# Kernel tuning notes

Measured on AMD Instinct MI355X. Metric: run time of the kernel, lower is better.

Reference implementation:

```python
import jax, jax.numpy as jnp
import numpy as np

B, C, K, N = 16, 512, 64, 8192
STAGE_NUM = 3


def setup_inputs() -> dict:
    key = jax.random.key(0)
    k0, k1, k2, k3 = jax.random.split(key, 4)
    x = jax.random.normal(k0, (B, C, N), jnp.float32)
    # conv1: Conv1d(c, c, 1) with bias; weight init N(0, sqrt(2/c))
    w1 = jax.random.normal(k1, (C, C), jnp.float32) * np.float32(np.sqrt(2.0 / C))
    b1 = jnp.zeros((C,), jnp.float32)
    # conv2: Conv1d(c, c, 1, bias=False) + BatchNorm1d(c) (gamma=1, beta=0)
    w2 = jax.random.normal(k2, (C, C), jnp.float32) * np.float32(np.sqrt(2.0 / C))
    gamma = jnp.ones((C,), jnp.float32)
    beta = jnp.zeros((C,), jnp.float32)
    # mu buffer: (1, c, k), N(0, sqrt(2/k)); is_normalized=False so no l2norm
    mu0 = jax.random.normal(k3, (1, C, K), jnp.float32) * np.float32(np.sqrt(2.0 / K))
    return {"x": x, "w1": w1, "b1": b1, "mu0": mu0, "w2": w2, "gamma": gamma, "beta": beta}


def reference(x, w1, b1, mu0, w2, gamma, beta):
    idn = x                                             # B,C,N
    # conv1 (1x1 conv == per-point matmul)
    x1 = jnp.einsum('oc,bcn->bon', w1, x) + b1[None, :, None]
    # EM iterations run under torch.no_grad() -> stop_gradient
    xs = jax.lax.stop_gradient(x1)
    mu = jnp.broadcast_to(mu0, (x.shape[0], C, K))      # B,C,K (buffer, no grad)
    z = None
    for _ in range(STAGE_NUM):
        z = jax.nn.softmax(jnp.einsum('bcn,bck->bnk', xs, mu), axis=2)  # E-step
        z_ = z / (1e-6 + z.sum(axis=1, keepdims=True))                  # normalize over N
        mu = jnp.einsum('bcn,bnk->bck', xs, z_)                         # M-step
        # is_normalized=False -> _l2norm is identity
    # reconstruction: mu @ z^T, relu
    x2 = jax.nn.relu(jnp.einsum('bck,bnk->bcn', mu, z))
    # conv2 (1x1, no bias) + BatchNorm1d (training-mode batch stats, eps=1e-5)
    x3 = jnp.einsum('oc,bcn->bon', w2, x2)
    mean = x3.mean(axis=(0, 2), keepdims=True)
    var = x3.var(axis=(0, 2), keepdims=True)
    y = gamma[None, :, None] * (x3 - mean) * jax.lax.rsqrt(var + 1e-5) + beta[None, :, None]
    out = y + idn
    return (out, mu)
```

## Files before the change

kernel.cpp:

```cpp
#include <hip/hip_runtime.h>
#include <math.h>

constexpr int B_ = 16, C_ = 512, K_ = 64, N_ = 8192;
constexpr int BHALF = 8;
constexpr int BGRP = 8;
constexpr int MCHUNK = 512;

typedef __bf16 bf16;
typedef __bf16 bf16x4 __attribute__((ext_vector_type(4)));
typedef __bf16 bf16x8 __attribute__((ext_vector_type(8)));
typedef float f32x4 __attribute__((ext_vector_type(4)));

#define GLDS16(gp, lp)                                              \
  __builtin_amdgcn_global_load_lds(                                 \
      (const __attribute__((address_space(1))) unsigned int*)(gp),  \
      (__attribute__((address_space(3))) unsigned int*)(lp), 16, 0, 0)

__device__ __forceinline__ bf16 lo_part(float v, bf16 h) {
  return (bf16)(v - (float)h);
}

__global__ __launch_bounds__(256) void transpose_split_x(
    const float* __restrict__ X, bf16* __restrict__ XTH, bf16* __restrict__ XTL) {
  const int b = blockIdx.z, c0 = blockIdx.y * 64, n0 = blockIdx.x * 64;
  __shared__ float tile[64][65];
  const int tid = threadIdx.x;
  const int rr = tid >> 4, q4 = (tid & 15) << 2;
#pragma unroll
  for (int r = 0; r < 4; ++r) {
    const int c = r * 16 + rr;
    *reinterpret_cast<float4*>(&tile[c][q4]) = *reinterpret_cast<const float4*>(
        &X[((size_t)b * C_ + c0 + c) * N_ + n0 + q4]);
  }
  __syncthreads();
#pragma unroll
  for (int r = 0; r < 4; ++r) {
    const int n = r * 16 + rr;
    bf16x4 oh, ol;
#pragma unroll
    for (int e = 0; e < 4; ++e) {
      const float v = tile[q4 + e][n];
      const bf16 h = (bf16)v;
      oh[e] = h;
      ol[e] = lo_part(v, h);
    }
    const size_t off = ((size_t)b * N_ + n0 + n) * C_ + c0 + q4;
    *reinterpret_cast<bf16x4*>(&XTH[off]) = oh;
    *reinterpret_cast<bf16x4*>(&XTL[off]) = ol;
  }
}

__global__ void cast_w_split(const float* __restrict__ W, bf16* __restrict__ H,
                             bf16* __restrict__ L) {
  const int i = blockIdx.x * 256 + threadIdx.x;
  const float v = W[i];
  const bf16 h = (bf16)v;
  H[i] = h;
  L[i] = lo_part(v, h);
}

__global__ void cast_mu0T_split(const float* __restrict__ MU0,
                                bf16* __restrict__ H, bf16* __restrict__ L) {
  const int k = blockIdx.x;
  for (int c = threadIdx.x; c < C_; c += 256) {
    const float v = MU0[c * K_ + k];
    const bf16 h = (bf16)v;
    H[k * C_ + c] = h;
    L[k * C_ + c] = lo_part(v, h);
  }
}

__global__ __launch_bounds__(256) void conv1_split(
    const bf16* __restrict__ XTH, const bf16* __restrict__ XTL,
    const bf16* __restrict__ W1H, const bf16* __restrict__ W1L,
    const float* __restrict__ bias, bf16* __restrict__ XSH,
    bf16* __restrict__ XSL) {
  const int bz = blockIdx.z;
  const int m0 = blockIdx.x * 128, n0 = blockIdx.y * 128;
  const bf16* __restrict__ AH = XTH + (size_t)bz * N_ * C_;
  const bf16* __restrict__ AL = XTL + (size_t)bz * N_ * C_;

  __shared__ bf16 SM[4 * 128 * 64];
  bf16* Ah = SM;
  bf16* Al = SM + 8192;
  bf16* Bh = SM + 16384;
  bf16* Bl = SM + 24576;

  const int tid = threadIdx.x, wid = tid >> 6, lane = tid & 63;
  const int lc = lane & 15, hi = lane >> 4;
  const int wm = wid >> 1, wn = wid & 1;
  const int swz = lc & 7;

  f32x4 acc[4][4] = {};

  for (int k0 = 0; k0 < C_; k0 += 64) {
#pragma unroll
    for (int it = 0; it < 4; ++it) {
      const int chunk = it * 256 + tid;
      const int row = chunk >> 3;
      const int koff = (((chunk & 7) ^ (row & 7)) << 3);
      const size_t doff = (size_t)(it * 256 + wid * 64) * 8;
      GLDS16(AH + (size_t)(m0 + row) * C_ + k0 + koff, Ah + doff);
      GLDS16(AL + (size_t)(m0 + row) * C_ + k0 + koff, Al + doff);
      GLDS16(W1H + (size_t)(n0 + row) * C_ + k0 + koff, Bh + doff);
      GLDS16(W1L + (size_t)(n0 + row) * C_ + k0 + koff, Bl + doff);
    }
    __syncthreads();
#pragma unroll
    for (int ks = 0; ks < 2; ++ks) {
      bf16x8 ah[4], al4[4], bh[4], bl4[4];
      const int kc = (((ks << 2) + hi) ^ swz) << 3;
#pragma unroll
      for (int i = 0; i < 4; ++i) {
        ah[i] = *reinterpret_cast<const bf16x8*>(Ah + (wm * 64 + i * 16 + lc) * 64 + kc);
        al4[i] = *reinterpret_cast<const bf16x8*>(Al + (wm * 64 + i * 16 + lc) * 64 + kc);
      }
#pragma unroll
      for (int j = 0; j < 4; ++j) {
        bh[j] = *reinterpret_cast<const bf16x8*>(Bh + (wn * 64 + j * 16 + lc) * 64 + kc);
        bl4[j] = *reinterpret_cast<const bf16x8*>(Bl + (wn * 64 + j * 16 + lc) * 64 + kc);
      }
#pragma unroll
      for (int i = 0; i < 4; ++i)
#pragma unroll
        for (int j = 0; j < 4; ++j) {
          acc[i][j] = __builtin_amdgcn_mfma_f32_16x16x32_bf16(al4[i], bh[j], acc[i][j], 0, 0, 0);
          acc[i][j] = __builtin_amdgcn_mfma_f32_16x16x32_bf16(ah[i], bl4[j], acc[i][j], 0, 0, 0);
          acc[i][j] = __builtin_amdgcn_mfma_f32_16x16x32_bf16(ah[i], bh[j], acc[i][j], 0, 0, 0);
        }
    }
    __syncthreads();
  }

  bf16 (*EP)[128] = reinterpret_cast<bf16(*)[128]>(SM);
  const int rr = tid >> 4, c8 = (tid & 15) << 3;
#pragma unroll
  for (int plane = 0; plane < 2; ++plane) {
    if (plane) __syncthreads();
#pragma unroll
    for (int j = 0; j < 4; ++j) {
      const int coll = wn * 64 + j * 16 + lc;
      const float bv = bias[n0 + coll];
#pragma unroll
      for (int i = 0; i < 4; ++i) {
        const int rowl = wm * 64 + i * 16 + hi * 4;
#pragma unroll
        for (int r = 0; r < 4; ++r) {
          const float v = acc[i][j][r] + bv;
          const bf16 h = (bf16)v;
          EP[rowl + r][coll] = plane ? lo_part(v, h) : h;
        }
      }
    }
    __syncthreads();
    bf16* DST = plane ? XSL : XSH;
#pragma unroll
    for (int rep = 0; rep < 8; ++rep) {
      const int row = rep * 16 + rr;
      *reinterpret_cast<bf16x8*>(&DST[((size_t)bz * N_ + m0 + row) * C_ + n0 + c8]) =
          *reinterpret_cast<const bf16x8*>(&EP[row][c8]);
    }
  }
}

__global__ __launch_bounds__(256) void estep_split(
    const bf16* __restrict__ XSH, const bf16* __restrict__ XSL,
    const bf16* __restrict__ MTH, const bf16* __restrict__ MTL,
    size_t mustride, bf16* __restrict__ ZH, bf16* __restrict__ ZL,
    float* __restrict__ colsum, int b_base) {
  const int b = b_base + blockIdx.y;
  const int m0 = blockIdx.x * 128;
  const bf16* __restrict__ AHp = XSH + (size_t)b * N_ * C_;
  const bf16* __restrict__ ALp = XSL + (size_t)b * N_ * C_;
  const bf16* __restrict__ BHp = MTH + (size_t)b * mustride;
  const bf16* __restrict__ BLp = MTL + (size_t)b * mustride;

  __shared__ bf16 Ah[128][64], Al[128][64], Bh[64][64], Bl[64][64];
  __shared__ float cs[64];

  const int tid = threadIdx.x, wid = tid >> 6, lane = tid & 63;
  const int lc = lane & 15, hi = lane >> 4;
  const int swz = lc & 7;
  if (tid < 64) cs[tid] = 0.0f;

  f32x4 acc[2][4] = {};
  for (int k0 = 0; k0 < C_; k0 += 64) {
#pragma unroll
    for (int it = 0; it < 4; ++it) {
      const int chunk = it * 256 + tid;
      const int row = chunk >> 3;
      const int koff = (((chunk & 7) ^ (row & 7)) << 3);
      const size_t doff = (size_t)(it * 256 + wid * 64) * 8;
      GLDS16(AHp + (size_t)(m0 + row) * C_ + k0 + koff, &Ah[0][0] + doff);
      GLDS16(ALp + (size_t)(m0 + row) * C_ + k0 + koff, &Al[0][0] + doff);
    }
#pragma unroll
    for (int it = 0; it < 2; ++it) {
      const int chunk = it * 256 + tid;
      const int row = chunk >> 3;
      const int koff = (((chunk & 7) ^ (row & 7)) << 3);
      const size_t doff = (size_t)(it * 256 + wid * 64) * 8;
      GLDS16(BHp + (size_t)row * C_ + k0 + koff, &Bh[0][0] + doff);
      GLDS16(BLp + (size_t)row * C_ + k0 + koff, &Bl[0][0] + doff);
    }
    __syncthreads();
#pragma unroll
    for (int ks = 0; ks < 2; ++ks) {
      const int kc = (((ks << 2) + hi) ^ swz) << 3;
      bf16x8 ah[2], al4[2], bh[4], bl4[4];
#pragma unroll
      for (int i = 0; i < 2; ++i) {
        ah[i] = *reinterpret_cast<const bf16x8*>(&Ah[wid * 32 + i * 16 + lc][kc]);
        al4[i] = *reinterpret_cast<const bf16x8*>(&Al[wid * 32 + i * 16 + lc][kc]);
      }
#pragma unroll
      for (int j = 0; j < 4; ++j) {
        bh[j] = *reinterpret_cast<const bf16x8*>(&Bh[j * 16 + lc][kc]);
        bl4[j] = *reinterpret_cast<const bf16x8*>(&Bl[j * 16 + lc][kc]);
      }
#pragma unroll
      for (int i = 0; i < 2; ++i)
#pragma unroll
        for (int j = 0; j < 4; ++j) {
          acc[i][j] = __builtin_amdgcn_mfma_f32_16x16x32_bf16(al4[i], bh[j], acc[i][j], 0, 0, 0);
          acc[i][j] = __builtin_amdgcn_mfma_f32_16x16x32_bf16(ah[i], bl4[j], acc[i][j], 0, 0, 0);
          acc[i][j] = __builtin_amdgcn_mfma_f32_16x16x32_bf16(ah[i], bh[j], acc[i][j], 0, 0, 0);
        }
    }
    __syncthreads();
  }

  float cp[4] = {0.f, 0.f, 0.f, 0.f};
#pragma unroll
  for (int i = 0; i < 2; ++i) {
#pragma unroll
    for (int r = 0; r < 4; ++r) {
      float v0 = acc[i][0][r], v1 = acc[i][1][r], v2 = acc[i][2][r], v3 = acc[i][3][r];
      float mx = fmaxf(fmaxf(v0, v1), fmaxf(v2, v3));
#pragma unroll
      for (int off = 1; off < 16; off <<= 1) mx = fmaxf(mx, __shfl_xor(mx, off));
      float p0 = __expf(v0 - mx), p1 = __expf(v1 - mx);
      float p2 = __expf(v2 - mx), p3 = __expf(v3 - mx);
      float s = p0 + p1 + p2 + p3;
#pragma unroll
      for (int off = 1; off < 16; off <<= 1) s += __shfl_xor(s, off);
      const float inv = 1.0f / s;
      p0 *= inv; p1 *= inv; p2 *= inv; p3 *= inv;
      const int n = m0 + wid * 32 + i * 16 + hi * 4 + r;
      bf16* zh = ZH + ((size_t)b * N_ + n) * K_;
      bf16* zl = ZL + ((size_t)b * N_ + n) * K_;
      const float pv[4] = {p0, p1, p2, p3};
#pragma unroll
      for (int j = 0; j < 4; ++j) {
        const bf16 h = (bf16)pv[j];
        zh[j * 16 + lc] = h;
        zl[j * 16 + lc] = lo_part(pv[j], h);
        cp[j] += pv[j];
      }
    }
  }
#pragma unroll
  for (int j = 0; j < 4; ++j) atomicAdd(&cs[j * 16 + lc], cp[j]);
  __syncthreads();
  if (tid < 64) atomicAdd(&colsum[b * K_ + tid], cs[tid]);
}

__global__ __launch_bounds__(128) void mstep_split(
    const bf16* __restrict__ XSH, const bf16* __restrict__ XSL,
    const bf16* __restrict__ ZHp, const bf16* __restrict__ ZLp,
    float* __restrict__ MUACC, int b_base) {
  const int b = b_base + blockIdx.z;
  const int c0 = blockIdx.y * 128;
  const int nbase = blockIdx.x * MCHUNK;
  const bf16* __restrict__ XbH = XSH + (size_t)b * N_ * C_;
  const bf16* __restrict__ XbL = XSL + (size_t)b * N_ * C_;
  const bf16* __restrict__ ZbH = ZHp + (size_t)b * N_ * K_;
  const bf16* __restrict__ ZbL = ZLp + (size_t)b * N_ * K_;

  __shared__ bf16 Ah[128][40], Al[128][40], Bh[64][40], Bl[64][40];

  const int tid = threadIdx.x, wid = tid >> 6, lane = tid & 63;
  const int lc = lane & 15, hi = lane >> 4;

  f32x4 acc[4][4] = {};
  for (int n0 = nbase; n0 < nbase + MCHUNK; n0 += 32) {
#pragma unroll
    for (int it = 0; it < 4; ++it) {
      const int chunk = it * 128 + tid;
      const int nn = chunk & 31, c8 = (chunk >> 5) * 8;
      const bf16x8 vh = *reinterpret_cast<const bf16x8*>(
          &XbH[(size_t)(n0 + nn) * C_ + c0 + c8]);
      const bf16x8 vl = *reinterpret_cast<const bf16x8*>(
          &XbL[(size_t)(n0 + nn) * C_ + c0 + c8]);
#pragma unroll
      for (int e = 0; e < 8; ++e) {
        Ah[c8 + e][nn] = vh[e];
        Al[c8 + e][nn] = vl[e];
      }
    }
#pragma unroll
    for (int it = 0; it < 2; ++it) {
      const int chunk = it * 128 + tid;
      const int nn = chunk & 31, k8 = (chunk >> 5) * 8;
      const bf16x8 vh = *reinterpret_cast<const bf16x8*>(
          &ZbH[(size_t)(n0 + nn) * K_ + k8]);
      const bf16x8 vl = *reinterpret_cast<const bf16x8*>(
          &ZbL[(size_t)(n0 + nn) * K_ + k8]);
#pragma unroll
      for (int e = 0; e < 8; ++e) {
        Bh[k8 + e][nn] = vh[e];
        Bl[k8 + e][nn] = vl[e];
      }
    }
    __syncthreads();
    bf16x8 ah[4], al4[4], bh[4], bl4[4];
#pragma unroll
    for (int i = 0; i < 4; ++i) {
      ah[i] = *reinterpret_cast<const bf16x8*>(&Ah[wid * 64 + i * 16 + lc][hi * 8]);
      al4[i] = *reinterpret_cast<const bf16x8*>(&Al[wid * 64 + i * 16 + lc][hi * 8]);
    }
#pragma unroll
    for (int j = 0; j < 4; ++j) {
      bh[j] = *reinterpret_cast<const bf16x8*>(&Bh[j * 16 + lc][hi * 8]);
      bl4[j] = *reinterpret_cast<const bf16x8*>(&Bl[j * 16 + lc][hi * 8]);
    }
#pragma unroll
    for (int i = 0; i < 4; ++i)
#pragma unroll
      for (int j = 0; j < 4; ++j) {
        acc[i][j] = __builtin_amdgcn_mfma_f32_16x16x32_bf16(al4[i], bh[j], acc[i][j], 0, 0, 0);
        acc[i][j] = __builtin_amdgcn_mfma_f32_16x16x32_bf16(ah[i], bl4[j], acc[i][j], 0, 0, 0);
        acc[i][j] = __builtin_amdgcn_mfma_f32_16x16x32_bf16(ah[i], bh[j], acc[i][j], 0, 0, 0);
      }
    __syncthreads();
  }
#pragma unroll
  for (int i = 0; i < 4; ++i) {
    const int c = c0 + wid * 64 + i * 16 + hi * 4;
#pragma unroll
    for (int r = 0; r < 4; ++r)
#pragma unroll
      for (int j = 0; j < 4; ++j)
        atomicAdd(&MUACC[((size_t)b * C_ + c + r) * K_ + j * 16 + lc], acc[i][j][r]);
  }
}

__global__ void finalize_mu(const float* __restrict__ MUACC,
                            const float* __restrict__ colsum,
                            bf16* __restrict__ MUTH, bf16* __restrict__ MUTL,
                            bf16* __restrict__ MUH, float* __restrict__ muout,
                            int idx_base) {
  const int idx = idx_base + blockIdx.x * 256 + threadIdx.x;
  const int k = idx & (K_ - 1);
  const int c = (idx >> 6) & (C_ - 1);
  const int b = idx >> 15;
  const float v = MUACC[idx] / (1e-6f + colsum[b * K_ + k]);
  const bf16 h = (bf16)v;
  MUH[idx] = h;
  MUTH[((size_t)b * K_ + k) * C_ + c] = h;
  MUTL[((size_t)b * K_ + k) * C_ + c] = lo_part(v, h);
  if (muout) muout[idx] = v;
}

__global__ __launch_bounds__(256) void x2_plain(
    const bf16* __restrict__ ZHp, const bf16* __restrict__ MUHp,
    bf16* __restrict__ X2) {
  const int b = blockIdx.z;
  const int m0 = blockIdx.x * 128, n0 = blockIdx.y * 128;
  const bf16* __restrict__ Ab = ZHp + (size_t)b * N_ * K_;
  const bf16* __restrict__ Bb = MUHp + (size_t)b * C_ * K_;

  __shared__ bf16 SM[2 * 128 * 64];
  bf16* As = SM;
  bf16* Bs = SM + 8192;

  const int tid = threadIdx.x, wid = tid >> 6, lane = tid & 63;
  const int lc = lane & 15, hi = lane >> 4;
  const int wm = wid >> 1, wn = wid & 1;
  const int swz = lc & 7;

  f32x4 acc[4][4] = {};
#pragma unroll
  for (int it = 0; it < 4; ++it) {
    const int chunk = it * 256 + tid;
    const int row = chunk >> 3;
    const int koff = (((chunk & 7) ^ (row & 7)) << 3);
    const size_t doff = (size_t)(it * 256 + wid * 64) * 8;
    GLDS16(Ab + (size_t)(m0 + row) * K_ + koff, As + doff);
    GLDS16(Bb + (size_t)(n0 + row) * K_ + koff, Bs + doff);
  }
  __syncthreads();
#pragma unroll
  for (int ks = 0; ks < 2; ++ks) {
    const int kc = (((ks << 2) + hi) ^ swz) << 3;
    bf16x8 af[4], bg[4];
#pragma unroll
    for (int i = 0; i < 4; ++i)
      af[i] = *reinterpret_cast<const bf16x8*>(As + (wm * 64 + i * 16 + lc) * 64 + kc);
#pragma unroll
    for (int j = 0; j < 4; ++j)
      bg[j] = *reinterpret_cast<const bf16x8*>(Bs + (wn * 64 + j * 16 + lc) * 64 + kc);
#pragma unroll
    for (int i = 0; i < 4; ++i)
#pragma unroll
      for (int j = 0; j < 4; ++j)
        acc[i][j] = __builtin_amdgcn_mfma_f32_16x16x32_bf16(af[i], bg[j], acc[i][j], 0, 0, 0);
  }
  __syncthreads();

  bf16 (*EP)[128] = reinterpret_cast<bf16(*)[128]>(SM);
#pragma unroll
  for (int j = 0; j < 4; ++j) {
    const int coll = wn * 64 + j * 16 + lc;
#pragma unroll
    for (int i = 0; i < 4; ++i) {
      const int rowl = wm * 64 + i * 16 + hi * 4;
#pragma unroll
      for (int r = 0; r < 4; ++r)
        EP[rowl + r][coll] = (bf16)fmaxf(acc[i][j][r], 0.0f);
    }
  }
  __syncthreads();
  const int rr = tid >> 4, c8 = (tid & 15) << 3;
#pragma unroll
  for (int rep = 0; rep < 8; ++rep) {
    const int row = rep * 16 + rr;
    *reinterpret_cast<bf16x8*>(&X2[((size_t)b * N_ + m0 + row) * C_ + n0 + c8]) =
        *reinterpret_cast<const bf16x8*>(&EP[row][c8]);
  }
}

__global__ __launch_bounds__(256) void conv2_stats(
    const bf16* __restrict__ W2H, const bf16* __restrict__ X2,
    float* __restrict__ psumP, float* __restrict__ psqP) {
  const int b = blockIdx.z;
  const int m0 = blockIdx.x * 128, n0 = blockIdx.y * 128;
  const bf16* __restrict__ Bb = X2 + (size_t)b * N_ * C_;

  __shared__ bf16 As[128][64], Bs[128][64];
  __shared__ float s_sum[128], s_sq[128];

  const int tid = threadIdx.x, wid = tid >> 6, lane = tid & 63;
  const int lc = lane & 15, hi = lane >> 4;
  const int wm = wid >> 1, wn = wid & 1;
  const int swz = lc & 7;
  if (tid < 128) { s_sum[tid] = 0.0f; s_sq[tid] = 0.0f; }

  f32x4 acc[4][4] = {};
  for (int k0 = 0; k0 < C_; k0 += 64) {
#pragma unroll
    for (int it = 0; it < 4; ++it) {
      const int chunk = it * 256 + tid;
      const int row = chunk >> 3;
      const int koff = (((chunk & 7) ^ (row & 7)) << 3);
      const size_t doff = (size_t)(it * 256 + wid * 64) * 8;
      GLDS16(W2H + (size_t)(m0 + row) * C_ + k0 + koff, &As[0][0] + doff);
      GLDS16(Bb + (size_t)(n0 + row) * C_ + k0 + koff, &Bs[0][0] + doff);
    }
    __syncthreads();
#pragma unroll
    for (int ks = 0; ks < 2; ++ks) {
      const int kc = (((ks << 2) + hi) ^ swz) << 3;
      bf16x8 af[4], bg[4];
#pragma unroll
      for (int i = 0; i < 4; ++i)
        af[i] = *reinterpret_cast<const bf16x8*>(&As[wm * 64 + i * 16 + lc][kc]);
#pragma unroll
      for (int j = 0; j < 4; ++j)
        bg[j] = *reinterpret_cast<const bf16x8*>(&Bs[wn * 64 + j * 16 + lc][kc]);
#pragma unroll
      for (int i = 0; i < 4; ++i)
#pragma unroll
        for (int j = 0; j < 4; ++j)
          acc[i][j] = __builtin_amdgcn_mfma_f32_16x16x32_bf16(af[i], bg[j], acc[i][j], 0, 0, 0);
    }
    __syncthreads();
  }

  float ps[4][4] = {};
  float pq[4][4] = {};
#pragma unroll
  for (int j = 0; j < 4; ++j)
#pragma unroll
    for (int i = 0; i < 4; ++i)
#pragma unroll
      for (int r = 0; r < 4; ++r) {
        const float v = acc[i][j][r];
        ps[i][r] += v;
        pq[i][r] += v * v;
      }
#pragma unroll
  for (int off = 1; off < 16; off <<= 1)
#pragma unroll
    for (int i = 0; i < 4; ++i)
#pragma unroll
      for (int r = 0; r < 4; ++r) {
        ps[i][r] += __shfl_xor(ps[i][r], off);
        pq[i][r] += __shfl_xor(pq[i][r], off);
      }
  if (lc == 0) {
#pragma unroll
    for (int i = 0; i < 4; ++i) {
      const int chl = wm * 64 + i * 16 + hi * 4;
#pragma unroll
      for (int r = 0; r < 4; ++r) {
        atomicAdd(&s_sum[chl + r], ps[i][r]);
        atomicAdd(&s_sq[chl + r], pq[i][r]);
      }
    }
  }
  __syncthreads();
  const int p = b * 64 + blockIdx.y;
  if (tid < 128) {
    psumP[(size_t)p * C_ + m0 + tid] = s_sum[tid];
    psqP[(size_t)p * C_ + m0 + tid] = s_sq[tid];
  }
}

__global__ __launch_bounds__(256) void bn_finalize2(
    const float* __restrict__ psumP, const float* __restrict__ psqP,
    const float* __restrict__ gamma, const float* __restrict__ beta,
    float* __restrict__ gc, float* __restrict__ oc) {
  const int c = blockIdx.x;
  const int tid = threadIdx.x;
  float s = 0.0f, q = 0.0f;
  for (int p = tid; p < B_ * 64; p += 256) {
    s += psumP[(size_t)p * C_ + c];
    q += psqP[(size_t)p * C_ + c];
  }
  __shared__ float ls[256], lq[256];
  ls[tid] = s;
  lq[tid] = q;
  __syncthreads();
  for (int off = 128; off > 0; off >>= 1) {
    if (tid < off) { ls[tid] += ls[tid + off]; lq[tid] += lq[tid + off]; }
    __syncthreads();
  }
  if (tid == 0) {
    const float inv = 1.0f / ((float)B_ * N_);
    const float mean = ls[0] * inv;
    const float var = lq[0] * inv - mean * mean;
    const float rstd = rsqrtf(var + 1e-5f);
    const float g = gamma[c] * rstd;
    gc[c] = g;
    oc[c] = beta[c] - mean * g;
  }
}

__global__ __launch_bounds__(256) void conv2_bn(
    const bf16* __restrict__ W2H, const bf16* __restrict__ X2,
    const float* __restrict__ gc, const float* __restrict__ oc,
    const float* __restrict__ Xin, float* __restrict__ OUT) {
  const int b = blockIdx.z;
  const int m0 = blockIdx.x * 128, n0 = blockIdx.y * 128;
  const bf16* __restrict__ Bb = X2 + (size_t)b * N_ * C_;

  __shared__ bf16 SM[2 * 128 * 64];
  bf16* As = SM;
  bf16* Bs = SM + 8192;

  const int tid = threadIdx.x, wid = tid >> 6, lane = tid & 63;
  const int lc = lane & 15, hi = lane >> 4;
  const int wm = wid >> 1, wn = wid & 1;
  const int swz = lc & 7;

  f32x4 acc[4][4] = {};
  for (int k0 = 0; k0 < C_; k0 += 64) {
#pragma unroll
    for (int it = 0; it < 4; ++it) {
      const int chunk = it * 256 + tid;
      const int row = chunk >> 3;
      const int koff = (((chunk & 7) ^ (row & 7)) << 3);
      const size_t doff = (size_t)(it * 256 + wid * 64) * 8;
      GLDS16(W2H + (size_t)(m0 + row) * C_ + k0 + koff, As + doff);
      GLDS16(Bb + (size_t)(n0 + row) * C_ + k0 + koff, Bs + doff);
    }
    __syncthreads();
#pragma unroll
    for (int ks = 0; ks < 2; ++ks) {
      const int kc = (((ks << 2) + hi) ^ swz) << 3;
      bf16x8 af[4], bg[4];
#pragma unroll
      for (int i = 0; i < 4; ++i)
        af[i] = *reinterpret_cast<const bf16x8*>(As + (wm * 64 + i * 16 + lc) * 64 + kc);
#pragma unroll
      for (int j = 0; j < 4; ++j)
        bg[j] = *reinterpret_cast<const bf16x8*>(Bs + (wn * 64 + j * 16 + lc) * 64 + kc);
#pragma unroll
      for (int i = 0; i < 4; ++i)
#pragma unroll
        for (int j = 0; j < 4; ++j)
          acc[i][j] = __builtin_amdgcn_mfma_f32_16x16x32_bf16(af[i], bg[j], acc[i][j], 0, 0, 0);
    }
    __syncthreads();
  }

  float (*EPF)[132] = reinterpret_cast<float(*)[132]>(SM);
  const int rr = tid >> 3, c4 = (tid & 7) << 2;
#pragma unroll
  for (int i = 0; i < 4; ++i) {
    if (i) __syncthreads();
    const int row0 = m0 + wm * 64 + i * 16 + hi * 4;
    const float4 g4 = *reinterpret_cast<const float4*>(&gc[row0]);
    const float4 o4 = *reinterpret_cast<const float4*>(&oc[row0]);
    const float ga[4] = {g4.x, g4.y, g4.z, g4.w};
    const float oa[4] = {o4.x, o4.y, o4.z, o4.w};
#pragma unroll
    for (int j = 0; j < 4; ++j) {
      const int coll = wn * 64 + j * 16 + lc;
#pragma unroll
      for (int r = 0; r < 4; ++r)
        EPF[wm * 16 + hi * 4 + r][coll] = acc[i][j][r] * ga[r] + oa[r];
    }
    __syncthreads();
    const int m = m0 + (rr >> 4) * 64 + i * 16 + (rr & 15);
#pragma unroll
    for (int rep = 0; rep < 4; ++rep) {
      const int col = rep * 32 + c4;
      const size_t off = ((size_t)b * C_ + m) * N_ + n0 + col;
      const float4 xi = *reinterpret_cast<const float4*>(&Xin[off]);
      float4 ov;
      ov.x = EPF[rr][col + 0] + xi.x;
      ov.y = EPF[rr][col + 1] + xi.y;
      ov.z = EPF[rr][col + 2] + xi.z;
      ov.w = EPF[rr][col + 3] + xi.w;
      *reinterpret_cast<float4*>(&OUT[off]) = ov;
    }
  }
}

extern "C" void kernel_launch(void* const* d_in, const int* in_sizes, int n_in,
                              void* d_out, int out_size, void* d_ws,
                              size_t ws_size, hipStream_t stream) {
  (void)in_sizes; (void)n_in; (void)out_size; (void)ws_size;
  const float* x     = (const float*)d_in[0];
  const float* w1    = (const float*)d_in[1];
  const float* b1    = (const float*)d_in[2];
  const float* mu0   = (const float*)d_in[3];
  const float* w2    = (const float*)d_in[4];
  const float* gamma = (const float*)d_in[5];
  const float* beta  = (const float*)d_in[6];

  bf16* XSH = (bf16*)d_out;
  bf16* XSL = XSH + (size_t)B_ * N_ * C_;
  float* OUT = (float*)d_out;
  float* MUOUT = OUT + (size_t)B_ * C_ * N_;

  bf16* XTH = (bf16*)d_ws;
  bf16* XTL = XTH + (size_t)BHALF * N_ * C_;
  bf16* X2b = XTH;
  bf16* ZH  = XTH + (size_t)B_ * N_ * C_;
  bf16* ZL  = ZH + (size_t)B_ * N_ * K_;
  bf16* W1H = ZL + (size_t)B_ * N_ * K_;
  bf16* W1L = W1H + C_ * C_;
  bf16* W2H = W1L + C_ * C_;
  bf16* W2L = W2H + C_ * C_;
  bf16* MT0H = W2L + C_ * C_;
  bf16* MT0L = MT0H + K_ * C_;
  bf16* MUTH = MT0L + K_ * C_;
  bf16* MUTL = MUTH + (size_t)B_ * K_ * C_;
  bf16* MUH  = MUTL + (size_t)B_ * K_ * C_;
  float* MUACC = (float*)(MUH + (size_t)B_ * C_ * K_);
  float* colsum = MUACC + (size_t)B_ * C_ * K_;
  float* gcp = colsum + B_ * K_;
  float* ocp = gcp + C_;
  float* psumP = ocp + C_;
  float* psqP  = psumP + (size_t)B_ * 64 * C_;

  const dim3 blk(256);

  cast_w_split<<<dim3(C_ * C_ / 256), blk, 0, stream>>>(w1, W1H, W1L);
  cast_w_split<<<dim3(C_ * C_ / 256), blk, 0, stream>>>(w2, W2H, W2L);
  cast_mu0T_split<<<dim3(K_), blk, 0, stream>>>(mu0, MT0H, MT0L);

  for (int half = 0; half < 2; ++half) {
    const float* xh = x + (size_t)half * BHALF * C_ * N_;
    transpose_split_x<<<dim3(N_ / 64, C_ / 64, BHALF), blk, 0, stream>>>(xh, XTH, XTL);
    conv1_split<<<dim3(N_ / 128, C_ / 128, BHALF), blk, 0, stream>>>(
        XTH, XTL, W1H, W1L, b1,
        XSH + (size_t)half * BHALF * N_ * C_, XSL + (size_t)half * BHALF * N_ * C_);
  }

  for (int g = 0; g < B_ / BGRP; ++g) {
    const int boff = g * BGRP;
    for (int it = 0; it < 3; ++it) {
      hipMemsetAsync(colsum + boff * K_, 0, BGRP * K_ * sizeof(float), stream);
      estep_split<<<dim3(N_ / 128, BGRP), blk, 0, stream>>>(
          XSH, XSL, it == 0 ? MT0H : MUTH, it == 0 ? MT0L : MUTL,
          it == 0 ? 0 : (size_t)K_ * C_, ZH, ZL, colsum, boff);
      hipMemsetAsync(MUACC + (size_t)boff * C_ * K_, 0,
                     (size_t)BGRP * C_ * K_ * sizeof(float), stream);
      mstep_split<<<dim3(N_ / MCHUNK, C_ / 128, BGRP), dim3(128), 0, stream>>>(
          XSH, XSL, ZH, ZL, MUACC, boff);
      finalize_mu<<<dim3(BGRP * C_ * K_ / 256), blk, 0, stream>>>(
          MUACC, colsum, MUTH, MUTL, MUH, it == 2 ? MUOUT : nullptr,
          boff * C_ * K_);
    }
  }

  x2_plain<<<dim3(N_ / 128, C_ / 128, B_), blk, 0, stream>>>(ZH, MUH, X2b);
  conv2_stats<<<dim3(C_ / 128, N_ / 128, B_), blk, 0, stream>>>(
      W2H, X2b, psumP, psqP);
  bn_finalize2<<<dim3(C_), blk, 0, stream>>>(psumP, psqP, gamma, beta, gcp, ocp);
  conv2_bn<<<dim3(C_ / 128, N_ / 128, B_), blk, 0, stream>>>(
      W2H, X2b, gcp, ocp, x, OUT);
}
```

Baseline: 1.164 ms.

## Compute conv2 GEMM once, storing pre-BN output, then apply BN elementwise in place

The conv2 GEMM used to run twice: once to gather BatchNorm statistics and once to apply the normalization and residual. Now the stats kernel also writes the fp32 pre-normalization result into the output buffer. A grid-stride elementwise kernel then applies scale, shift and the residual in place. Separately, finalize_mu zeroes MUACC after reading it, replacing the per-iteration memsets with one memset up front. This trades a second GEMM for an extra fp32 write and re-read of the full output tensor, so it adds memory traffic in return for less compute.

```diff
diff --git a/kernel.cpp b/kernel.cpp
--- a/kernel.cpp
+++ b/kernel.cpp
@@ -345,7 +345,7 @@
   }
 }
 
-__global__ void finalize_mu(const float* __restrict__ MUACC,
+__global__ void finalize_mu(float* __restrict__ MUACC,
                             const float* __restrict__ colsum,
                             bf16* __restrict__ MUTH, bf16* __restrict__ MUTL,
                             bf16* __restrict__ MUH, float* __restrict__ muout,
@@ -355,6 +355,7 @@
   const int c = (idx >> 6) & (C_ - 1);
   const int b = idx >> 15;
   const float v = MUACC[idx] / (1e-6f + colsum[b * K_ + k]);
+  MUACC[idx] = 0.0f;
   const bf16 h = (bf16)v;
   MUH[idx] = h;
   MUTH[((size_t)b * K_ + k) * C_ + c] = h;
@@ -430,14 +431,17 @@
   }
 }
 
-__global__ __launch_bounds__(256) void conv2_stats(
+__global__ __launch_bounds__(256) void conv2_full(
     const bf16* __restrict__ W2H, const bf16* __restrict__ X2,
-    float* __restrict__ psumP, float* __restrict__ psqP) {
+    float* __restrict__ psumP, float* __restrict__ psqP,
+    float* __restrict__ X3out) {
   const int b = blockIdx.z;
   const int m0 = blockIdx.x * 128, n0 = blockIdx.y * 128;
   const bf16* __restrict__ Bb = X2 + (size_t)b * N_ * C_;
 
-  __shared__ bf16 As[128][64], Bs[128][64];
+  __shared__ bf16 SM[2 * 128 * 64];
+  bf16* As = SM;
+  bf16* Bs = SM + 8192;
   __shared__ float s_sum[128], s_sq[128];
 
   const int tid = threadIdx.x, wid = tid >> 6, lane = tid & 63;
@@ -454,8 +458,8 @@
       const int row = chunk >> 3;
       const int koff = (((chunk & 7) ^ (row & 7)) << 3);
       const size_t doff = (size_t)(it * 256 + wid * 64) * 8;
-      GLDS16(W2H + (size_t)(m0 + row) * C_ + k0 + koff, &As[0][0] + doff);
-      GLDS16(Bb + (size_t)(n0 + row) * C_ + k0 + koff, &Bs[0][0] + doff);
+      GLDS16(W2H + (size_t)(m0 + row) * C_ + k0 + koff, As + doff);
+      GLDS16(Bb + (size_t)(n0 + row) * C_ + k0 + koff, Bs + doff);
     }
     __syncthreads();
 #pragma unroll
@@ -464,10 +468,10 @@
       bf16x8 af[4], bg[4];
 #pragma unroll
       for (int i = 0; i < 4; ++i)
-        af[i] = *reinterpret_cast<const bf16x8*>(&As[wm * 64 + i * 16 + lc][kc]);
+        af[i] = *reinterpret_cast<const bf16x8*>(As + (wm * 64 + i * 16 + lc) * 64 + kc);
 #pragma unroll
       for (int j = 0; j < 4; ++j)
-        bg[j] = *reinterpret_cast<const bf16x8*>(&Bs[wn * 64 + j * 16 + lc][kc]);
+        bg[j] = *reinterpret_cast<const bf16x8*>(Bs + (wn * 64 + j * 16 + lc) * 64 + kc);
 #pragma unroll
       for (int i = 0; i < 4; ++i)
 #pragma unroll
@@ -509,7 +513,34 @@
       }
     }
   }
-  __syncthreads();
+
+  float (*EPF)[132] = reinterpret_cast<float(*)[132]>(SM);
+  const int rr = tid >> 3, c4 = (tid & 7) << 2;
+#pragma unroll
+  for (int i = 0; i < 4; ++i) {
+    __syncthreads();
+#pragma unroll
+    for (int j = 0; j < 4; ++j) {
+      const int coll = wn * 64 + j * 16 + lc;
+#pragma unroll
+      for (int r = 0; r < 4; ++r)
+        EPF[wm * 16 + hi * 4 + r][coll] = acc[i][j][r];
+    }
+    __syncthreads();
+    const int m = m0 + (rr >> 4) * 64 + i * 16 + (rr & 15);
+#pragma unroll
+    for (int rep = 0; rep < 4; ++rep) {
+      const int col = rep * 32 + c4;
+      const size_t off = ((size_t)b * C_ + m) * N_ + n0 + col;
+      float4 ov;
+      ov.x = EPF[rr][col + 0];
+      ov.y = EPF[rr][col + 1];
+      ov.z = EPF[rr][col + 2];
+      ov.w = EPF[rr][col + 3];
+      *reinterpret_cast<float4*>(&X3out[off]) = ov;
+    }
+  }
+
   const int p = b * 64 + blockIdx.y;
   if (tid < 128) {
     psumP[(size_t)p * C_ + m0 + tid] = s_sum[tid];
@@ -547,85 +578,22 @@
   }
 }
 
-__global__ __launch_bounds__(256) void conv2_bn(
-    const bf16* __restrict__ W2H, const bf16* __restrict__ X2,
-    const float* __restrict__ gc, const float* __restrict__ oc,
-    const float* __restrict__ Xin, float* __restrict__ OUT) {
-  const int b = blockIdx.z;
-  const int m0 = blockIdx.x * 128, n0 = blockIdx.y * 128;
-  const bf16* __restrict__ Bb = X2 + (size_t)b * N_ * C_;
-
-  __shared__ bf16 SM[2 * 128 * 64];
-  bf16* As = SM;
-  bf16* Bs = SM + 8192;
-
-  const int tid = threadIdx.x, wid = tid >> 6, lane = tid & 63;
-  const int lc = lane & 15, hi = lane >> 4;
-  const int wm = wid >> 1, wn = wid & 1;
-  const int swz = lc & 7;
-
-  f32x4 acc[4][4] = {};
-  for (int k0 = 0; k0 < C_; k0 += 64) {
-#pragma unroll
-    for (int it = 0; it < 4; ++it) {
-      const int chunk = it * 256 + tid;
-      const int row = chunk >> 3;
-      const int koff = (((chunk & 7) ^ (row & 7)) << 3);
-      const size_t doff = (size_t)(it * 256 + wid * 64) * 8;
-      GLDS16(W2H + (size_t)(m0 + row) * C_ + k0 + koff, As + doff);
-      GLDS16(Bb + (size_t)(n0 + row) * C_ + k0 + koff, Bs + doff);
-    }
-    __syncthreads();
-#pragma unroll
-    for (int ks = 0; ks < 2; ++ks) {
-      const int kc = (((ks << 2) + hi) ^ swz) << 3;
-      bf16x8 af[4], bg[4];
-#pragma unroll
-      for (int i = 0; i < 4; ++i)
-        af[i] = *reinterpret_cast<const bf16x8*>(As + (wm * 64 + i * 16 + lc) * 64 + kc);
-#pragma unroll
-      for (int j = 0; j < 4; ++j)
-        bg[j] = *reinterpret_cast<const bf16x8*>(Bs + (wn * 64 + j * 16 + lc) * 64 + kc);
-#pragma unroll
-      for (int i = 0; i < 4; ++i)
-#pragma unroll
-        for (int j = 0; j < 4; ++j)
-          acc[i][j] = __builtin_amdgcn_mfma_f32_16x16x32_bf16(af[i], bg[j], acc[i][j], 0, 0, 0);
-    }
-    __syncthreads();
-  }
-
-  float (*EPF)[132] = reinterpret_cast<float(*)[132]>(SM);
-  const int rr = tid >> 3, c4 = (tid & 7) << 2;
-#pragma unroll
-  for (int i = 0; i < 4; ++i) {
-    if (i) __syncthreads();
-    const int row0 = m0 + wm * 64 + i * 16 + hi * 4;
-    const float4 g4 = *reinterpret_cast<const float4*>(&gc[row0]);
-    const float4 o4 = *reinterpret_cast<const float4*>(&oc[row0]);
-    const float ga[4] = {g4.x, g4.y, g4.z, g4.w};
-    const float oa[4] = {o4.x, o4.y, o4.z, o4.w};
-#pragma unroll
-    for (int j = 0; j < 4; ++j) {
-      const int coll = wn * 64 + j * 16 + lc;
-#pragma unroll
-      for (int r = 0; r < 4; ++r)
-        EPF[wm * 16 + hi * 4 + r][coll] = acc[i][j][r] * ga[r] + oa[r];
-    }
-    __syncthreads();
-    const int m = m0 + (rr >> 4) * 64 + i * 16 + (rr & 15);
-#pragma unroll
-    for (int rep = 0; rep < 4; ++rep) {
-      const int col = rep * 32 + c4;
-      const size_t off = ((size_t)b * C_ + m) * N_ + n0 + col;
-      const float4 xi = *reinterpret_cast<const float4*>(&Xin[off]);
-      float4 ov;
-      ov.x = EPF[rr][col + 0] + xi.x;
-      ov.y = EPF[rr][col + 1] + xi.y;
-      ov.z = EPF[rr][col + 2] + xi.z;
-      ov.w = EPF[rr][col + 3] + xi.w;
-      *reinterpret_cast<float4*>(&OUT[off]) = ov;
-    }
+__global__ __launch_bounds__(256) void bn_inplace(
+    float* __restrict__ OUT, const float* __restrict__ Xin,
+    const float* __restrict__ gc, const float* __restrict__ oc) {
+  const size_t total4 = (size_t)B_ * C_ * N_ / 4;
+  for (size_t i = (size_t)blockIdx.x * 256 + threadIdx.x; i < total4;
+       i += (size_t)gridDim.x * 256) {
+    const int c = (int)((i >> 11) & (C_ - 1));
+    const float g = gc[c];
+    const float o = oc[c];
+    float4 v = reinterpret_cast<const float4*>(OUT)[i];
+    const float4 xi = reinterpret_cast<const float4*>(Xin)[i];
+    v.x = v.x * g + o + xi.x;
+    v.y = v.y * g + o + xi.y;
+    v.z = v.z * g + o + xi.z;
+    v.w = v.w * g + o + xi.w;
+    reinterpret_cast<float4*>(OUT)[i] = v;
   }
 }
 
@@ -672,6 +640,7 @@
   cast_w_split<<<dim3(C_ * C_ / 256), blk, 0, stream>>>(w1, W1H, W1L);
   cast_w_split<<<dim3(C_ * C_ / 256), blk, 0, stream>>>(w2, W2H, W2L);
   cast_mu0T_split<<<dim3(K_), blk, 0, stream>>>(mu0, MT0H, MT0L);
+  hipMemsetAsync(MUACC, 0, (size_t)B_ * C_ * K_ * sizeof(float), stream);
 
   for (int half = 0; half < 2; ++half) {
     const float* xh = x + (size_t)half * BHALF * C_ * N_;
@@ -688,8 +657,6 @@
       estep_split<<<dim3(N_ / 128, BGRP), blk, 0, stream>>>(
           XSH, XSL, it == 0 ? MT0H : MUTH, it == 0 ? MT0L : MUTL,
           it == 0 ? 0 : (size_t)K_ * C_, ZH, ZL, colsum, boff);
-      hipMemsetAsync(MUACC + (size_t)boff * C_ * K_, 0,
-                     (size_t)BGRP * C_ * K_ * sizeof(float), stream);
       mstep_split<<<dim3(N_ / MCHUNK, C_ / 128, BGRP), dim3(128), 0, stream>>>(
           XSH, XSL, ZH, ZL, MUACC, boff);
       finalize_mu<<<dim3(BGRP * C_ * K_ / 256), blk, 0, stream>>>(
@@ -699,9 +666,8 @@
   }
 
   x2_plain<<<dim3(N_ / 128, C_ / 128, B_), blk, 0, stream>>>(ZH, MUH, X2b);
-  conv2_stats<<<dim3(C_ / 128, N_ / 128, B_), blk, 0, stream>>>(
-      W2H, X2b, psumP, psqP);
+  conv2_full<<<dim3(C_ / 128, N_ / 128, B_), blk, 0, stream>>>(
+      W2H, X2b, psumP, psqP, OUT);
   bn_finalize2<<<dim3(C_), blk, 0, stream>>>(psumP, psqP, gamma, beta, gcp, ocp);
-  conv2_bn<<<dim3(C_ / 128, N_ / 128, B_), blk, 0, stream>>>(
-      W2H, X2b, gcp, ocp, x, OUT);
-}
+  bn_inplace<<<dim3(2048), blk, 0, stream>>>(OUT, x, gcp, ocp);
+}
```

Result: slower. 1.201 ms (+3.1%).

## Fuse x transpose and bf16 split into conv1, zero MUACC in finalize

Applied to the files above, without the earlier changes.

Drops the separate transpose_split_x pass. conv1 now reads fp32 x tiles straight into LDS and converts them to hi/lo bf16 in registers before the MFMAs, which avoids writing and re-reading the transposed split copies of x. Separately, finalize_mu now zeroes MUACC after reading it, so the per-iteration memsets are replaced by one memset up front. The cost is that conv1 performs the conversion per tile with scalar strided LDS reads and an extra barrier per k-subblock, and the A operand no longer uses the async global-to-LDS path.

```diff
diff --git a/kernel.cpp b/kernel.cpp
--- a/kernel.cpp
+++ b/kernel.cpp
@@ -2,7 +2,6 @@
 #include <math.h>
 
 constexpr int B_ = 16, C_ = 512, K_ = 64, N_ = 8192;
-constexpr int BHALF = 8;
 constexpr int BGRP = 8;
 constexpr int MCHUNK = 512;
 
@@ -18,36 +17,6 @@
 
 __device__ __forceinline__ bf16 lo_part(float v, bf16 h) {
   return (bf16)(v - (float)h);
-}
-
-__global__ __launch_bounds__(256) void transpose_split_x(
-    const float* __restrict__ X, bf16* __restrict__ XTH, bf16* __restrict__ XTL) {
-  const int b = blockIdx.z, c0 = blockIdx.y * 64, n0 = blockIdx.x * 64;
-  __shared__ float tile[64][65];
-  const int tid = threadIdx.x;
-  const int rr = tid >> 4, q4 = (tid & 15) << 2;
-#pragma unroll
-  for (int r = 0; r < 4; ++r) {
-    const int c = r * 16 + rr;
-    *reinterpret_cast<float4*>(&tile[c][q4]) = *reinterpret_cast<const float4*>(
-        &X[((size_t)b * C_ + c0 + c) * N_ + n0 + q4]);
-  }
-  __syncthreads();
-#pragma unroll
-  for (int r = 0; r < 4; ++r) {
-    const int n = r * 16 + rr;
-    bf16x4 oh, ol;
-#pragma unroll
-    for (int e = 0; e < 4; ++e) {
-      const float v = tile[q4 + e][n];
-      const bf16 h = (bf16)v;
-      oh[e] = h;
-      ol[e] = lo_part(v, h);
-    }
-    const size_t off = ((size_t)b * N_ + n0 + n) * C_ + c0 + q4;
-    *reinterpret_cast<bf16x4*>(&XTH[off]) = oh;
-    *reinterpret_cast<bf16x4*>(&XTL[off]) = ol;
-  }
 }
 
 __global__ void cast_w_split(const float* __restrict__ W, bf16* __restrict__ H,
@@ -70,26 +39,25 @@
   }
 }
 
-__global__ __launch_bounds__(256) void conv1_split(
-    const bf16* __restrict__ XTH, const bf16* __restrict__ XTL,
-    const bf16* __restrict__ W1H, const bf16* __restrict__ W1L,
-    const float* __restrict__ bias, bf16* __restrict__ XSH,
-    bf16* __restrict__ XSL) {
+__global__ __launch_bounds__(256) void conv1_fused(
+    const float* __restrict__ X, const bf16* __restrict__ W1H,
+    const bf16* __restrict__ W1L, const float* __restrict__ bias,
+    bf16* __restrict__ XSH, bf16* __restrict__ XSL) {
   const int bz = blockIdx.z;
-  const int m0 = blockIdx.x * 128, n0 = blockIdx.y * 128;
-  const bf16* __restrict__ AH = XTH + (size_t)bz * N_ * C_;
-  const bf16* __restrict__ AL = XTL + (size_t)bz * N_ * C_;
-
-  __shared__ bf16 SM[4 * 128 * 64];
-  bf16* Ah = SM;
-  bf16* Al = SM + 8192;
-  bf16* Bh = SM + 16384;
-  bf16* Bl = SM + 24576;
+  const int m0 = blockIdx.x * 128;
+  const int n0 = blockIdx.y * 128;
+  const float* __restrict__ Xb = X + (size_t)bz * C_ * N_;
+
+  __shared__ float Xs32[32 * 130];
+  __shared__ bf16 Bbuf[2 * 128 * 64];
+  bf16* Bh = Bbuf;
+  bf16* Bl = Bbuf + 8192;
 
   const int tid = threadIdx.x, wid = tid >> 6, lane = tid & 63;
   const int lc = lane & 15, hi = lane >> 4;
   const int wm = wid >> 1, wn = wid & 1;
   const int swz = lc & 7;
+  const int srow = tid >> 3, scolg = (tid & 7) << 4;
 
   f32x4 acc[4][4] = {};
 
@@ -100,39 +68,55 @@
       const int row = chunk >> 3;
       const int koff = (((chunk & 7) ^ (row & 7)) << 3);
       const size_t doff = (size_t)(it * 256 + wid * 64) * 8;
-      GLDS16(AH + (size_t)(m0 + row) * C_ + k0 + koff, Ah + doff);
-      GLDS16(AL + (size_t)(m0 + row) * C_ + k0 + koff, Al + doff);
       GLDS16(W1H + (size_t)(n0 + row) * C_ + k0 + koff, Bh + doff);
       GLDS16(W1L + (size_t)(n0 + row) * C_ + k0 + koff, Bl + doff);
     }
-    __syncthreads();
-#pragma unroll
-    for (int ks = 0; ks < 2; ++ks) {
-      bf16x8 ah[4], al4[4], bh[4], bl4[4];
-      const int kc = (((ks << 2) + hi) ^ swz) << 3;
-#pragma unroll
-      for (int i = 0; i < 4; ++i) {
-        ah[i] = *reinterpret_cast<const bf16x8*>(Ah + (wm * 64 + i * 16 + lc) * 64 + kc);
-        al4[i] = *reinterpret_cast<const bf16x8*>(Al + (wm * 64 + i * 16 + lc) * 64 + kc);
-      }
-#pragma unroll
-      for (int j = 0; j < 4; ++j) {
-        bh[j] = *reinterpret_cast<const bf16x8*>(Bh + (wn * 64 + j * 16 + lc) * 64 + kc);
-        bl4[j] = *reinterpret_cast<const bf16x8*>(Bl + (wn * 64 + j * 16 + lc) * 64 + kc);
-      }
-#pragma unroll
-      for (int i = 0; i < 4; ++i)
+#pragma unroll
+    for (int sub = 0; sub < 2; ++sub) {
+      {
+        const float* src = &Xb[(size_t)(k0 + sub * 32 + srow) * N_ + m0 + scolg];
+        float* dstb = &Xs32[srow * 130 + scolg];
+#pragma unroll
+        for (int q = 0; q < 4; ++q) {
+          const float4 v = *reinterpret_cast<const float4*>(src + q * 4);
+          *reinterpret_cast<float2*>(dstb + q * 4) = make_float2(v.x, v.y);
+          *reinterpret_cast<float2*>(dstb + q * 4 + 2) = make_float2(v.z, v.w);
+        }
+      }
+      __syncthreads();
+      {
+        bf16x8 ah[4], al4[4], bh[4], bl4[4];
+        const int kc = (((sub << 2) + hi) ^ swz) << 3;
+#pragma unroll
+        for (int i = 0; i < 4; ++i) {
+          const int arow = wm * 64 + i * 16 + lc;
+#pragma unroll
+          for (int e = 0; e < 8; ++e) {
+            const float v = Xs32[(hi * 8 + e) * 130 + arow];
+            const bf16 h = (bf16)v;
+            ah[i][e] = h;
+            al4[i][e] = lo_part(v, h);
+          }
+        }
 #pragma unroll
         for (int j = 0; j < 4; ++j) {
-          acc[i][j] = __builtin_amdgcn_mfma_f32_16x16x32_bf16(al4[i], bh[j], acc[i][j], 0, 0, 0);
-          acc[i][j] = __builtin_amdgcn_mfma_f32_16x16x32_bf16(ah[i], bl4[j], acc[i][j], 0, 0, 0);
-          acc[i][j] = __builtin_amdgcn_mfma_f32_16x16x32_bf16(ah[i], bh[j], acc[i][j], 0, 0, 0);
+          bh[j] = *reinterpret_cast<const bf16x8*>(Bh + (wn * 64 + j * 16 + lc) * 64 + kc);
+          bl4[j] = *reinterpret_cast<const bf16x8*>(Bl + (wn * 64 + j * 16 + lc) * 64 + kc);
         }
-    }
-    __syncthreads();
-  }
-
-  bf16 (*EP)[128] = reinterpret_cast<bf16(*)[128]>(SM);
+#pragma unroll
+        for (int i = 0; i < 4; ++i)
+#pragma unroll
+          for (int j = 0; j < 4; ++j) {
+            acc[i][j] = __builtin_amdgcn_mfma_f32_16x16x32_bf16(al4[i], bh[j], acc[i][j], 0, 0, 0);
+            acc[i][j] = __builtin_amdgcn_mfma_f32_16x16x32_bf16(ah[i], bl4[j], acc[i][j], 0, 0, 0);
+            acc[i][j] = __builtin_amdgcn_mfma_f32_16x16x32_bf16(ah[i], bh[j], acc[i][j], 0, 0, 0);
+          }
+      }
+      __syncthreads();
+    }
+  }
+
+  bf16 (*EP)[128] = reinterpret_cast<bf16(*)[128]>(Bbuf);
   const int rr = tid >> 4, c8 = (tid & 15) << 3;
 #pragma unroll
   for (int plane = 0; plane < 2; ++plane) {
@@ -345,7 +329,7 @@
   }
 }
 
-__global__ void finalize_mu(const float* __restrict__ MUACC,
+__global__ void finalize_mu(float* __restrict__ MUACC,
                             const float* __restrict__ colsum,
                             bf16* __restrict__ MUTH, bf16* __restrict__ MUTL,
                             bf16* __restrict__ MUH, float* __restrict__ muout,
@@ -355,6 +339,7 @@
   const int c = (idx >> 6) & (C_ - 1);
   const int b = idx >> 15;
   const float v = MUACC[idx] / (1e-6f + colsum[b * K_ + k]);
+  MUACC[idx] = 0.0f;
   const bf16 h = (bf16)v;
   MUH[idx] = h;
   MUTH[((size_t)b * K_ + k) * C_ + c] = h;
@@ -646,10 +631,8 @@
   float* OUT = (float*)d_out;
   float* MUOUT = OUT + (size_t)B_ * C_ * N_;
 
-  bf16* XTH = (bf16*)d_ws;
-  bf16* XTL = XTH + (size_t)BHALF * N_ * C_;
-  bf16* X2b = XTH;
-  bf16* ZH  = XTH + (size_t)B_ * N_ * C_;
+  bf16* X2b = (bf16*)d_ws;
+  bf16* ZH  = X2b + (size_t)B_ * N_ * C_;
   bf16* ZL  = ZH + (size_t)B_ * N_ * K_;
   bf16* W1H = ZL + (size_t)B_ * N_ * K_;
   bf16* W1L = W1H + C_ * C_;
@@ -672,14 +655,10 @@
   cast_w_split<<<dim3(C_ * C_ / 256), blk, 0, stream>>>(w1, W1H, W1L);
   cast_w_split<<<dim3(C_ * C_ / 256), blk, 0, stream>>>(w2, W2H, W2L);
   cast_mu0T_split<<<dim3(K_), blk, 0, stream>>>(mu0, MT0H, MT0L);
-
-  for (int half = 0; half < 2; ++half) {
-    const float* xh = x + (size_t)half * BHALF * C_ * N_;
-    transpose_split_x<<<dim3(N_ / 64, C_ / 64, BHALF), blk, 0, stream>>>(xh, XTH, XTL);
-    conv1_split<<<dim3(N_ / 128, C_ / 128, BHALF), blk, 0, stream>>>(
-        XTH, XTL, W1H, W1L, b1,
-        XSH + (size_t)half * BHALF * N_ * C_, XSL + (size_t)half * BHALF * N_ * C_);
-  }
+  hipMemsetAsync(MUACC, 0, (size_t)B_ * C_ * K_ * sizeof(float), stream);
+
+  conv1_fused<<<dim3(N_ / 128, C_ / 128, B_), blk, 0, stream>>>(
+      x, W1H, W1L, b1, XSH, XSL);
 
   for (int g = 0; g < B_ / BGRP; ++g) {
     const int boff = g * BGRP;
@@ -688,8 +667,6 @@
       estep_split<<<dim3(N_ / 128, BGRP), blk, 0, stream>>>(
           XSH, XSL, it == 0 ? MT0H : MUTH, it == 0 ? MT0L : MUTL,
           it == 0 ? 0 : (size_t)K_ * C_, ZH, ZL, colsum, boff);
-      hipMemsetAsync(MUACC + (size_t)boff * C_ * K_, 0,
-                     (size_t)BGRP * C_ * K_ * sizeof(float), stream);
       mstep_split<<<dim3(N_ / MCHUNK, C_ / 128, BGRP), dim3(128), 0, stream>>>(
           XSH, XSL, ZH, ZL, MUACC, boff);
       finalize_mu<<<dim3(BGRP * C_ * K_ / 256), blk, 0, stream>>>(
```

New measurement: 1.153 ms. Within noise of the previous version (-1.0%).
